# Optimization experiments

Hardware: AMD Instinct MI355X
Metric: run time of the kernel (lower is better)

## Reference

```python
import jax, jax.numpy as jnp
import numpy as np

S1, S2, B, H, E, IN, OUT, NL = 8, 32, 256, 1024, 512, 2, 2, 4


def setup_inputs() -> dict:
    key = jax.random.key(0)
    ks = jax.random.split(key, 20)
    s_h = 1.0 / np.sqrt(H)
    inp = {
        'input': jax.random.normal(ks[0], (B, IN), jnp.float32),
        'h0': jax.random.normal(ks[1], (NL, B, H), jnp.float32) * 0.5,
        'c0': jax.random.normal(ks[2], (NL, B, H), jnp.float32) * 0.5,
        'all_outputs': jax.random.normal(ks[3], (S1, S2, B, H), jnp.float32),
        'W_emb': jax.random.normal(ks[4], (E, IN), jnp.float32) / np.sqrt(IN),
        'b_emb': jax.random.normal(ks[5], (E,), jnp.float32) * 0.01,
        'W_attn': jax.random.normal(ks[6], (1, 2 * H), jnp.float32) / np.sqrt(2 * H),
        'b_attn': jax.random.normal(ks[7], (1,), jnp.float32) * 0.01,
        'Wih0': jax.random.normal(ks[8], (4 * H, E + H), jnp.float32) / np.sqrt(E + H),
        'Whh0': jax.random.normal(ks[9], (4 * H, H), jnp.float32) * s_h,
        'bih0': jax.random.normal(ks[10], (4 * H,), jnp.float32) * 0.01,
        'bhh0': jax.random.normal(ks[11], (4 * H,), jnp.float32) * 0.01,
        'Wih_r': jax.random.normal(ks[12], (NL - 1, 4 * H, H), jnp.float32) * s_h,
        'Whh_r': jax.random.normal(ks[13], (NL - 1, 4 * H, H), jnp.float32) * s_h,
        'bih_r': jax.random.normal(ks[14], (NL - 1, 4 * H), jnp.float32) * 0.01,
        'bhh_r': jax.random.normal(ks[15], (NL - 1, 4 * H), jnp.float32) * 0.01,
        'W_out': jax.random.normal(ks[16], (OUT, H), jnp.float32) * s_h,
        'b_out': jax.random.normal(ks[17], (OUT,), jnp.float32) * 0.01,
    }
    return inp


def _lstm_cell(x, h, c, Wih, Whh, bih, bhh):
    g = x @ Wih.T + h @ Whh.T + bih + bhh  # [B, 4H], torch gate order i,f,g,o
    i, f, gg, o = jnp.split(g, 4, axis=1)
    c2 = jax.nn.sigmoid(f) * c + jax.nn.sigmoid(i) * jnp.tanh(gg)
    h2 = jax.nn.sigmoid(o) * jnp.tanh(c2)
    return h2, c2


def reference(input, h0, c0, all_outputs, W_emb, b_emb, W_attn, b_attn,
              Wih0, Whh0, bih0, bhh0, Wih_r, Whh_r, bih_r, bhh_r, W_out, b_out):
    s1, s2, b, h_dim = all_outputs.shape
    # embedding (dropout = identity in eval mode)
    embedded = jax.nn.relu(input @ W_emb.T + b_emb)  # [B, E]
    h_top = h0[0]  # [B, H]
    # attn(cat(h_top, y)) decomposed: h part is shared across all (j, i)
    w_h = W_attn[0, :h_dim]
    w_y = W_attn[0, h_dim:]
    scores = (jnp.einsum('jibh,h->jib', all_outputs, w_y)
              + (h_top @ w_h)[None, None, :] + b_attn[0])  # [S1, S2, B]
    # torch cats per-(j,i) [B,1] columns j-major -> [B, S1*S2]
    normalized = jax.nn.softmax(scores.reshape(s1 * s2, b).T, axis=1)  # [B, S1*S2]
    temp = normalized.reshape(b, s1, s2)
    # NOTE: original writes into an expand()-ed zero buffer, so every j-slice
    # aliases the same memory; after the loop all slices equal the last j's bmm
    # result and sum(0) multiplies it by S1. We replicate that exactly.
    applied_last = jnp.einsum('bi,ibh->bh', temp[:, -1, :], all_outputs[-1])  # [B, H]
    final_attn = s1 * applied_last
    x = jnp.concatenate([final_attn, embedded], axis=1)  # [B, H+E]
    hs, cs = [], []
    h, c = _lstm_cell(x, h0[0], c0[0], Wih0, Whh0, bih0, bhh0)
    hs.append(h); cs.append(c)
    for l in range(Wih_r.shape[0]):  # inter-layer dropout = identity in eval
        h, c = _lstm_cell(h, h0[l + 1], c0[l + 1], Wih_r[l], Whh_r[l], bih_r[l], bhh_r[l])
        hs.append(h); cs.append(c)
    h_new = jnp.stack(hs)
    c_new = jnp.stack(cs)
    final_output = h @ W_out.T + b_out  # [B, OUT]
    return final_output, h_new, c_new, normalized
```

## Files before the change

kernel.cpp:

```cpp
#include <hip/hip_runtime.h>
#include <hip/hip_bf16.h>

typedef __bf16 bf16x8 __attribute__((ext_vector_type(8)));
typedef __bf16 bf16x4 __attribute__((ext_vector_type(4)));
typedef float  f32x4  __attribute__((ext_vector_type(4)));

#define O_FINAL 0
#define O_H     512
#define O_C     1049088
#define O_NORM  2097664

__device__ __forceinline__ bf16x8 cvt8(float4 a, float4 b) {
  bf16x8 r;
  r[0] = (__bf16)a.x; r[1] = (__bf16)a.y; r[2] = (__bf16)a.z; r[3] = (__bf16)a.w;
  r[4] = (__bf16)b.x; r[5] = (__bf16)b.y; r[6] = (__bf16)b.z; r[7] = (__bf16)b.w;
  return r;
}

template<int K>
__device__ __forceinline__ void tile_gemm_ff(const float* __restrict__ A,
                                             const float* __restrict__ W,
                                             int r0, int j0,
                                             __bf16* __restrict__ At,
                                             __bf16* __restrict__ Wt,
                                             f32x4 acc[2]) {
  const int t = threadIdx.x, lane = t & 63, wave = t >> 6;
  const int rf = wave & 3, gg = wave >> 2;
  const int tr = t >> 3, chunk = t & 7;
  const float* wsrc = W + (size_t)((tr >> 4) * 1024 + j0 + (tr & 15)) * K + chunk * 8;
  const float* asrc = A + (size_t)(r0 + tr) * K + chunk * 8;
  const int sw_off = (chunk ^ (tr & 7)) << 4;
  char* wdst = (char*)Wt + tr * 128 + sw_off;
  char* adst = (char*)At + tr * 128 + sw_off;
  const int a_tr  = rf * 16 + (lane & 15);
  const int w_tr0 = gg * 32 + (lane & 15);
  const int w_tr1 = w_tr0 + 16;
  const int ksel  = lane >> 4;

  float4 wr0 = *(const float4*)wsrc, wr1 = *(const float4*)(wsrc + 4);
  float4 ar0 = *(const float4*)asrc, ar1 = *(const float4*)(asrc + 4);

  constexpr int NK = K / 64;
#pragma unroll 2
  for (int step = 0; step < NK; ++step) {
    __syncthreads();
    *(bf16x8*)wdst = cvt8(wr0, wr1);
    *(bf16x8*)adst = cvt8(ar0, ar1);
    __syncthreads();
    if (step + 1 < NK) {
      wr0 = *(const float4*)(wsrc + (step + 1) * 64);
      wr1 = *(const float4*)(wsrc + (step + 1) * 64 + 4);
      ar0 = *(const float4*)(asrc + (step + 1) * 64);
      ar1 = *(const float4*)(asrc + (step + 1) * 64 + 4);
    }
#pragma unroll
    for (int s = 0; s < 2; ++s) {
      const int chk = s * 4 + ksel;
      bf16x8 af  = *(const bf16x8*)((char*)At + a_tr  * 128 + ((chk ^ (a_tr  & 7)) << 4));
      bf16x8 wf0 = *(const bf16x8*)((char*)Wt + w_tr0 * 128 + ((chk ^ (w_tr0 & 7)) << 4));
      bf16x8 wf1 = *(const bf16x8*)((char*)Wt + w_tr1 * 128 + ((chk ^ (w_tr1 & 7)) << 4));
      acc[0] = __builtin_amdgcn_mfma_f32_16x16x32_bf16(af, wf0, acc[0], 0, 0, 0);
      acc[1] = __builtin_amdgcn_mfma_f32_16x16x32_bf16(af, wf1, acc[1], 0, 0, 0);
    }
  }
}

template<int K>
__device__ __forceinline__ void tile_gemm_bb(const __bf16* __restrict__ A,
                                             const __bf16* __restrict__ W,
                                             int r0, int j0,
                                             __bf16* __restrict__ At,
                                             __bf16* __restrict__ Wt,
                                             f32x4 acc[2]) {
  const int t = threadIdx.x, lane = t & 63, wave = t >> 6;
  const int rf = wave & 3, gg = wave >> 2;
  const int tr = t >> 3, chunk = t & 7;
  const __bf16* wsrc = W + (size_t)((tr >> 4) * 1024 + j0 + (tr & 15)) * K + chunk * 8;
  const __bf16* asrc = A + (size_t)(r0 + tr) * K + chunk * 8;
  const int sw_off = (chunk ^ (tr & 7)) << 4;
  char* wdst = (char*)Wt + tr * 128 + sw_off;
  char* adst = (char*)At + tr * 128 + sw_off;
  const int a_tr  = rf * 16 + (lane & 15);
  const int w_tr0 = gg * 32 + (lane & 15);
  const int w_tr1 = w_tr0 + 16;
  const int ksel  = lane >> 4;

  bf16x8 wr = *(const bf16x8*)wsrc;
  bf16x8 ar = *(const bf16x8*)asrc;

  constexpr int NK = K / 64;
#pragma unroll 2
  for (int step = 0; step < NK; ++step) {
    __syncthreads();
    *(bf16x8*)wdst = wr;
    *(bf16x8*)adst = ar;
    __syncthreads();
    if (step + 1 < NK) {
      wr = *(const bf16x8*)(wsrc + (step + 1) * 64);
      ar = *(const bf16x8*)(asrc + (step + 1) * 64);
    }
#pragma unroll
    for (int s = 0; s < 2; ++s) {
      const int chk = s * 4 + ksel;
      bf16x8 af  = *(const bf16x8*)((char*)At + a_tr  * 128 + ((chk ^ (a_tr  & 7)) << 4));
      bf16x8 wf0 = *(const bf16x8*)((char*)Wt + w_tr0 * 128 + ((chk ^ (w_tr0 & 7)) << 4));
      bf16x8 wf1 = *(const bf16x8*)((char*)Wt + w_tr1 * 128 + ((chk ^ (w_tr1 & 7)) << 4));
      acc[0] = __builtin_amdgcn_mfma_f32_16x16x32_bf16(af, wf0, acc[0], 0, 0, 0);
      acc[1] = __builtin_amdgcn_mfma_f32_16x16x32_bf16(af, wf1, acc[1], 0, 0, 0);
    }
  }
}

__global__ __launch_bounds__(512) void k_front(
    const float* __restrict__ AO, const float* __restrict__ Wattn,
    float* __restrict__ sc,
    const float* __restrict__ h0,
    const float* __restrict__ Whh0, const float* __restrict__ Whh_r,
    const float* __restrict__ bih0, const float* __restrict__ bhh0,
    const float* __restrict__ bih_r, const float* __restrict__ bhh_r,
    float* __restrict__ Gh,
    const float* __restrict__ Wih0, const float* __restrict__ Wih_r,
    __bf16* __restrict__ Wihb) {
  const int t = threadIdx.x, lane = t & 63, wave = t >> 6;
  if (blockIdx.x < 2048) {
    const float* wy = Wattn + 1024;
    float4 wv[4];
#pragma unroll
    for (int q = 0; q < 4; ++q) wv[q] = *(const float4*)(wy + lane * 4 + 256 * q);
    const int row0 = (blockIdx.x * 8 + wave) * 4;
    float a4[4];
#pragma unroll
    for (int rr = 0; rr < 4; ++rr) {
      const float4* rp = (const float4*)(AO + (size_t)(row0 + rr) * 1024);
      float a = 0.f;
#pragma unroll
      for (int q = 0; q < 4; ++q) {
        float4 v = rp[lane + 64 * q];
        a += v.x * wv[q].x + v.y * wv[q].y + v.z * wv[q].z + v.w * wv[q].w;
      }
      a4[rr] = a;
    }
#pragma unroll
    for (int rr = 0; rr < 4; ++rr) {
      float a = a4[rr];
#pragma unroll
      for (int off = 32; off; off >>= 1) a += __shfl_xor(a, off, 64);
      if (lane == 0) {
        int row = row0 + rr;
        sc[(row & 255) * 256 + (row >> 8)] = a;
      }
    }
    return;
  }
  if (blockIdx.x < 3072) {
    __shared__ __bf16 At[64 * 64];
    __shared__ __bf16 Wt[64 * 64];
    const int j = blockIdx.x - 2048;
    const int l = j >> 8, inner = j & 255;
    const int cb = inner & 63, rb = inner >> 6;
    const int j0 = cb * 16, r0 = rb * 64;
    const float* A  = h0 + (size_t)l * 262144;
    const float* W  = (l == 0) ? Whh0 : (Whh_r + (size_t)(l - 1) * 4194304);
    const float* bi = (l == 0) ? bih0 : (bih_r + (size_t)(l - 1) * 4096);
    const float* bh = (l == 0) ? bhh0 : (bhh_r + (size_t)(l - 1) * 4096);
    f32x4 acc[2] = {};
    tile_gemm_ff<1024>(A, W, r0, j0, At, Wt, acc);
    float* Go = Gh + (size_t)l * 1048576;
    const int rf = wave & 3, gg = wave >> 2;
    const int col = j0 + (lane & 15);
    const int rbase = r0 + rf * 16 + ((lane >> 4) << 2);
#pragma unroll
    for (int gi = 0; gi < 2; ++gi) {
      const int cg = (gg * 2 + gi) * 1024 + col;
#pragma unroll
      for (int q = 0; q < 4; ++q)
        Go[(size_t)(rbase + q) * 4096 + cg] = acc[gi][q] + bi[cg] + bh[cg];
    }
    return;
  }
  const int tid = ((int)blockIdx.x - 3072) * 512 + t;
#pragma unroll
  for (int n = 0; n < 8; ++n) {
    int idx = tid + n * 589824;
    float4 v = (idx < 1572864) ? ((const float4*)Wih0)[idx]
                               : ((const float4*)Wih_r)[idx - 1572864];
    bf16x4 o;
    o[0] = (__bf16)v.x; o[1] = (__bf16)v.y; o[2] = (__bf16)v.z; o[3] = (__bf16)v.w;
    ((bf16x4*)Wihb)[idx] = o;
  }
}

__global__ __launch_bounds__(256) void k_smx(const float* __restrict__ sc,
                                             const float* __restrict__ AO,
                                             const float* __restrict__ inp,
                                             const float* __restrict__ Wemb,
                                             const float* __restrict__ bemb,
                                             float* __restrict__ norm_out,
                                             __bf16* __restrict__ x) {
  __shared__ float red[4];
  __shared__ float wsm[32];
  const int b = blockIdx.x, t = threadIdx.x, lane = t & 63, wave = t >> 6;
  float s = sc[b * 256 + t];
  float m = s;
#pragma unroll
  for (int off = 32; off; off >>= 1) m = fmaxf(m, __shfl_xor(m, off, 64));
  if (lane == 0) red[wave] = m;
  __syncthreads();
  m = fmaxf(fmaxf(red[0], red[1]), fmaxf(red[2], red[3]));
  float e = __expf(s - m);
  float sum = e;
#pragma unroll
  for (int off = 32; off; off >>= 1) sum += __shfl_xor(sum, off, 64);
  __syncthreads();
  if (lane == 0) red[wave] = sum;
  __syncthreads();
  sum = red[0] + red[1] + red[2] + red[3];
  float nv = e / sum;
  norm_out[b * 256 + t] = nv;
  if (t >= 224) wsm[t - 224] = nv;
  __syncthreads();
  float acc[4] = {0.f, 0.f, 0.f, 0.f};
  const float* base = AO + ((size_t)224 * 256 + b) * 1024;
#pragma unroll 4
  for (int i = 0; i < 32; ++i) {
    float w = wsm[i];
    const float* rp = base + (size_t)i * 262144;
#pragma unroll
    for (int q = 0; q < 4; ++q) acc[q] += w * rp[t + 256 * q];
  }
#pragma unroll
  for (int q = 0; q < 4; ++q) x[(size_t)b * 1536 + t + 256 * q] = (__bf16)(8.0f * acc[q]);
  float i0 = inp[b * 2], i1 = inp[b * 2 + 1];
#pragma unroll
  for (int r = 0; r < 2; ++r) {
    int jj = t + 256 * r;
    float e2 = i0 * Wemb[jj * 2] + i1 * Wemb[jj * 2 + 1] + bemb[jj];
    x[(size_t)b * 1536 + 1024 + jj] = (__bf16)fmaxf(e2, 0.f);
  }
}

template<int K>
__global__ __launch_bounds__(512) void k_layer(const __bf16* __restrict__ A,
                                               const __bf16* __restrict__ Wb,
                                               const float* __restrict__ Gh,
                                               const float* __restrict__ c0l,
                                               float* __restrict__ h_out,
                                               float* __restrict__ c_out,
                                               __bf16* __restrict__ hb) {
  __shared__ __bf16 At[64 * 64];
  __shared__ __bf16 Wt[64 * 64];
  __shared__ float exch[4][2][256];
  const int t = threadIdx.x, lane = t & 63, wave = t >> 6;
  const int rf = wave & 3, gg = wave >> 2;
  const int cb = blockIdx.x & 63, rb = blockIdx.x >> 6;
  const int j0 = cb * 16, r0 = rb * 64;
  f32x4 acc[2] = {};
  tile_gemm_bb<K>(A, Wb, r0, j0, At, Wt, acc);
  const int col = j0 + (lane & 15);
  const int rbase = r0 + rf * 16 + ((lane >> 4) << 2);
#pragma unroll
  for (int gi = 0; gi < 2; ++gi) {
    const float* gp = Gh + (size_t)rbase * 4096 + (gg * 2 + gi) * 1024 + col;
#pragma unroll
    for (int q = 0; q < 4; ++q) acc[gi][q] += gp[(size_t)q * 4096];
  }
  const int eidx = ((lane >> 4) << 2) * 16 + (lane & 15);
  if (gg == 1) {
#pragma unroll
    for (int gi = 0; gi < 2; ++gi)
#pragma unroll
      for (int q = 0; q < 4; ++q)
        exch[rf][gi][eidx + q * 16] = acc[gi][q];
  }
  __syncthreads();
  if (gg == 0) {
#pragma unroll
    for (int q = 0; q < 4; ++q) {
      const int row = rbase + q;
      float gv = exch[rf][0][eidx + q * 16];
      float ov = exch[rf][1][eidx + q * 16];
      float si = 1.f / (1.f + __expf(-acc[0][q]));
      float sf = 1.f / (1.f + __expf(-acc[1][q]));
      float so = 1.f / (1.f + __expf(-ov));
      float c2 = sf * c0l[(size_t)row * 1024 + col] + si * tanhf(gv);
      float h2 = so * tanhf(c2);
      h_out[(size_t)row * 1024 + col] = h2;
      c_out[(size_t)row * 1024 + col] = c2;
      hb[(size_t)row * 1024 + col] = (__bf16)h2;
    }
  }
}

__global__ __launch_bounds__(256) void k_final(const float* __restrict__ h3,
                                               const float* __restrict__ Wout,
                                               const float* __restrict__ bout,
                                               float* __restrict__ out) {
  const int lane = threadIdx.x & 63, wave = threadIdx.x >> 6;
  const int b = blockIdx.x * 4 + wave;
  const float4* hp = (const float4*)(h3 + (size_t)b * 1024);
  const float4* w0 = (const float4*)Wout;
  const float4* w1 = (const float4*)(Wout + 1024);
  float a0 = 0.f, a1 = 0.f;
#pragma unroll
  for (int q = 0; q < 4; ++q) {
    float4 hv = hp[lane + 64 * q];
    float4 v0 = w0[lane + 64 * q];
    float4 v1 = w1[lane + 64 * q];
    a0 += hv.x * v0.x + hv.y * v0.y + hv.z * v0.z + hv.w * v0.w;
    a1 += hv.x * v1.x + hv.y * v1.y + hv.z * v1.z + hv.w * v1.w;
  }
#pragma unroll
  for (int off = 32; off; off >>= 1) {
    a0 += __shfl_xor(a0, off, 64);
    a1 += __shfl_xor(a1, off, 64);
  }
  if (lane == 0) {
    out[b * 2]     = a0 + bout[0];
    out[b * 2 + 1] = a1 + bout[1];
  }
}

extern "C" void kernel_launch(void* const* d_in, const int* in_sizes, int n_in,
                              void* d_out, int out_size, void* d_ws, size_t ws_size,
                              hipStream_t stream) {
  const float* inp    = (const float*)d_in[0];
  const float* h0     = (const float*)d_in[1];
  const float* c0     = (const float*)d_in[2];
  const float* AO     = (const float*)d_in[3];
  const float* Wemb   = (const float*)d_in[4];
  const float* bemb   = (const float*)d_in[5];
  const float* Wattn  = (const float*)d_in[6];
  const float* Wih0   = (const float*)d_in[8];
  const float* Whh0   = (const float*)d_in[9];
  const float* bih0   = (const float*)d_in[10];
  const float* bhh0   = (const float*)d_in[11];
  const float* Wih_r  = (const float*)d_in[12];
  const float* Whh_r  = (const float*)d_in[13];
  const float* bih_r  = (const float*)d_in[14];
  const float* bhh_r  = (const float*)d_in[15];
  const float* Wout   = (const float*)d_in[16];
  const float* bout   = (const float*)d_in[17];

  float* out = (float*)d_out;
  char* ws = (char*)d_ws;

  __bf16* Wihb  = (__bf16*)ws;
  float*  Gh    = (float*)(ws + 37748736);
  __bf16* xb    = (__bf16*)(ws + 54525952);
  __bf16* hb    = (__bf16*)(ws + 55312384);
  float*  sc    = (float*)(ws + 57409536);
  __bf16* Wihb0 = Wihb;
  __bf16* Wihbr = Wihb + 6291456;

  k_front<<<4224, 512, 0, stream>>>(AO, Wattn, sc, h0, Whh0, Whh_r,
                                    bih0, bhh0, bih_r, bhh_r, Gh,
                                    Wih0, Wih_r, Wihb);
  k_smx<<<256, 256, 0, stream>>>(sc, AO, inp, Wemb, bemb, out + O_NORM, xb);

  k_layer<1536><<<256, 512, 0, stream>>>(xb, Wihb0, Gh, c0,
                                         out + O_H, out + O_C, hb);
  for (int l = 1; l < 4; ++l)
    k_layer<1024><<<256, 512, 0, stream>>>(hb + (size_t)(l - 1) * 262144,
                                           Wihbr + (size_t)(l - 1) * 4194304,
                                           Gh + (size_t)l * 1048576,
                                           c0 + (size_t)l * 262144,
                                           out + O_H + (size_t)l * 262144,
                                           out + O_C + (size_t)l * 262144,
                                           hb + (size_t)l * 262144);

  k_final<<<64, 256, 0, stream>>>(out + O_H + 3 * 262144, Wout, bout, out + O_FINAL);
}
```

Before: 166.3 us.

## Double-buffer LDS tiles and prefetch four K-steps ahead in GEMM tiles

Reworks both tile GEMM helpers to use two LDS buffers with a single barrier per K-step, and keeps four register-staged global loads in flight instead of one. The goal is to hide global memory latency and drop one barrier per iteration in the recurrent-weight GEMM and the per-layer LSTM GEMMs. The cost is more registers for the prefetch slots and a larger shared buffer of 40 KB per block, which may reduce occupancy. The exch area now sits inside the shared buffer, so an extra barrier guards its reuse.

```diff
diff --git a/kernel.cpp b/kernel.cpp
--- a/kernel.cpp
+++ b/kernel.cpp
@@ -18,93 +18,101 @@
 }
 
 template<int K>
+__device__ __forceinline__ void tile_gemm_bb(const __bf16* __restrict__ A,
+                                             const __bf16* __restrict__ W,
+                                             int r0, int j0, char* lds,
+                                             f32x4 acc[2]) {
+  constexpr int NK = K / 64;
+  constexpr int D = 4;
+  const int t = threadIdx.x, lane = t & 63, wave = t >> 6;
+  const int rf = wave & 3, gg = wave >> 2;
+  const int tr = t >> 3, chunk = t & 7;
+  const __bf16* wsrc = W + (size_t)((tr >> 4) * 1024 + j0 + (tr & 15)) * K + chunk * 8;
+  const __bf16* asrc = A + (size_t)(r0 + tr) * K + chunk * 8;
+  const int sw_off = (chunk ^ (tr & 7)) << 4;
+  const int woff = 8192 + tr * 128 + sw_off;
+  const int aoff = tr * 128 + sw_off;
+  const int a_tr  = rf * 16 + (lane & 15);
+  const int w_tr0 = gg * 32 + (lane & 15);
+  const int w_tr1 = w_tr0 + 16;
+  const int ksel  = lane >> 4;
+
+  bf16x8 wp[D], ap[D];
+#pragma unroll
+  for (int d = 0; d < D; ++d) {
+    wp[d] = *(const bf16x8*)(wsrc + d * 64);
+    ap[d] = *(const bf16x8*)(asrc + d * 64);
+  }
+#pragma unroll
+  for (int s = 0; s < NK; ++s) {
+    const int sl = s % D;
+    char* buf = lds + (s & 1) * 16384;
+    *(bf16x8*)(buf + aoff) = ap[sl];
+    *(bf16x8*)(buf + woff) = wp[sl];
+    if (s + D < NK) {
+      wp[sl] = *(const bf16x8*)(wsrc + (s + D) * 64);
+      ap[sl] = *(const bf16x8*)(asrc + (s + D) * 64);
+    }
+    __syncthreads();
+#pragma unroll
+    for (int s2 = 0; s2 < 2; ++s2) {
+      const int chk = s2 * 4 + ksel;
+      bf16x8 af  = *(const bf16x8*)(buf + a_tr * 128 + ((chk ^ (a_tr & 7)) << 4));
+      bf16x8 wf0 = *(const bf16x8*)(buf + 8192 + w_tr0 * 128 + ((chk ^ (w_tr0 & 7)) << 4));
+      bf16x8 wf1 = *(const bf16x8*)(buf + 8192 + w_tr1 * 128 + ((chk ^ (w_tr1 & 7)) << 4));
+      acc[0] = __builtin_amdgcn_mfma_f32_16x16x32_bf16(af, wf0, acc[0], 0, 0, 0);
+      acc[1] = __builtin_amdgcn_mfma_f32_16x16x32_bf16(af, wf1, acc[1], 0, 0, 0);
+    }
+  }
+}
+
+template<int K>
 __device__ __forceinline__ void tile_gemm_ff(const float* __restrict__ A,
                                              const float* __restrict__ W,
-                                             int r0, int j0,
-                                             __bf16* __restrict__ At,
-                                             __bf16* __restrict__ Wt,
+                                             int r0, int j0, char* lds,
                                              f32x4 acc[2]) {
+  constexpr int NK = K / 64;
+  constexpr int D = 4;
   const int t = threadIdx.x, lane = t & 63, wave = t >> 6;
   const int rf = wave & 3, gg = wave >> 2;
   const int tr = t >> 3, chunk = t & 7;
   const float* wsrc = W + (size_t)((tr >> 4) * 1024 + j0 + (tr & 15)) * K + chunk * 8;
   const float* asrc = A + (size_t)(r0 + tr) * K + chunk * 8;
   const int sw_off = (chunk ^ (tr & 7)) << 4;
-  char* wdst = (char*)Wt + tr * 128 + sw_off;
-  char* adst = (char*)At + tr * 128 + sw_off;
+  const int woff = 8192 + tr * 128 + sw_off;
+  const int aoff = tr * 128 + sw_off;
   const int a_tr  = rf * 16 + (lane & 15);
   const int w_tr0 = gg * 32 + (lane & 15);
   const int w_tr1 = w_tr0 + 16;
   const int ksel  = lane >> 4;
 
-  float4 wr0 = *(const float4*)wsrc, wr1 = *(const float4*)(wsrc + 4);
-  float4 ar0 = *(const float4*)asrc, ar1 = *(const float4*)(asrc + 4);
-
-  constexpr int NK = K / 64;
-#pragma unroll 2
-  for (int step = 0; step < NK; ++step) {
+  float4 wp[D][2], ap[D][2];
+#pragma unroll
+  for (int d = 0; d < D; ++d) {
+    wp[d][0] = *(const float4*)(wsrc + d * 64);
+    wp[d][1] = *(const float4*)(wsrc + d * 64 + 4);
+    ap[d][0] = *(const float4*)(asrc + d * 64);
+    ap[d][1] = *(const float4*)(asrc + d * 64 + 4);
+  }
+#pragma unroll
+  for (int s = 0; s < NK; ++s) {
+    const int sl = s % D;
+    char* buf = lds + (s & 1) * 16384;
+    *(bf16x8*)(buf + aoff) = cvt8(ap[sl][0], ap[sl][1]);
+    *(bf16x8*)(buf + woff) = cvt8(wp[sl][0], wp[sl][1]);
+    if (s + D < NK) {
+      wp[sl][0] = *(const float4*)(wsrc + (s + D) * 64);
+      wp[sl][1] = *(const float4*)(wsrc + (s + D) * 64 + 4);
+      ap[sl][0] = *(const float4*)(asrc + (s + D) * 64);
+      ap[sl][1] = *(const float4*)(asrc + (s + D) * 64 + 4);
+    }
     __syncthreads();
-    *(bf16x8*)wdst = cvt8(wr0, wr1);
-    *(bf16x8*)adst = cvt8(ar0, ar1);
-    __syncthreads();
-    if (step + 1 < NK) {
-      wr0 = *(const float4*)(wsrc + (step + 1) * 64);
-      wr1 = *(const float4*)(wsrc + (step + 1) * 64 + 4);
-      ar0 = *(const float4*)(asrc + (step + 1) * 64);
-      ar1 = *(const float4*)(asrc + (step + 1) * 64 + 4);
-    }
-#pragma unroll
-    for (int s = 0; s < 2; ++s) {
-      const int chk = s * 4 + ksel;
-      bf16x8 af  = *(const bf16x8*)((char*)At + a_tr  * 128 + ((chk ^ (a_tr  & 7)) << 4));
-      bf16x8 wf0 = *(const bf16x8*)((char*)Wt + w_tr0 * 128 + ((chk ^ (w_tr0 & 7)) << 4));
-      bf16x8 wf1 = *(const bf16x8*)((char*)Wt + w_tr1 * 128 + ((chk ^ (w_tr1 & 7)) << 4));
-      acc[0] = __builtin_amdgcn_mfma_f32_16x16x32_bf16(af, wf0, acc[0], 0, 0, 0);
-      acc[1] = __builtin_amdgcn_mfma_f32_16x16x32_bf16(af, wf1, acc[1], 0, 0, 0);
-    }
-  }
-}
-
-template<int K>
-__device__ __forceinline__ void tile_gemm_bb(const __bf16* __restrict__ A,
-                                             const __bf16* __restrict__ W,
-                                             int r0, int j0,
-                                             __bf16* __restrict__ At,
-                                             __bf16* __restrict__ Wt,
-                                             f32x4 acc[2]) {
-  const int t = threadIdx.x, lane = t & 63, wave = t >> 6;
-  const int rf = wave & 3, gg = wave >> 2;
-  const int tr = t >> 3, chunk = t & 7;
-  const __bf16* wsrc = W + (size_t)((tr >> 4) * 1024 + j0 + (tr & 15)) * K + chunk * 8;
-  const __bf16* asrc = A + (size_t)(r0 + tr) * K + chunk * 8;
-  const int sw_off = (chunk ^ (tr & 7)) << 4;
-  char* wdst = (char*)Wt + tr * 128 + sw_off;
-  char* adst = (char*)At + tr * 128 + sw_off;
-  const int a_tr  = rf * 16 + (lane & 15);
-  const int w_tr0 = gg * 32 + (lane & 15);
-  const int w_tr1 = w_tr0 + 16;
-  const int ksel  = lane >> 4;
-
-  bf16x8 wr = *(const bf16x8*)wsrc;
-  bf16x8 ar = *(const bf16x8*)asrc;
-
-  constexpr int NK = K / 64;
-#pragma unroll 2
-  for (int step = 0; step < NK; ++step) {
-    __syncthreads();
-    *(bf16x8*)wdst = wr;
-    *(bf16x8*)adst = ar;
-    __syncthreads();
-    if (step + 1 < NK) {
-      wr = *(const bf16x8*)(wsrc + (step + 1) * 64);
-      ar = *(const bf16x8*)(asrc + (step + 1) * 64);
-    }
-#pragma unroll
-    for (int s = 0; s < 2; ++s) {
-      const int chk = s * 4 + ksel;
-      bf16x8 af  = *(const bf16x8*)((char*)At + a_tr  * 128 + ((chk ^ (a_tr  & 7)) << 4));
-      bf16x8 wf0 = *(const bf16x8*)((char*)Wt + w_tr0 * 128 + ((chk ^ (w_tr0 & 7)) << 4));
-      bf16x8 wf1 = *(const bf16x8*)((char*)Wt + w_tr1 * 128 + ((chk ^ (w_tr1 & 7)) << 4));
+#pragma unroll
+    for (int s2 = 0; s2 < 2; ++s2) {
+      const int chk = s2 * 4 + ksel;
+      bf16x8 af  = *(const bf16x8*)(buf + a_tr * 128 + ((chk ^ (a_tr & 7)) << 4));
+      bf16x8 wf0 = *(const bf16x8*)(buf + 8192 + w_tr0 * 128 + ((chk ^ (w_tr0 & 7)) << 4));
+      bf16x8 wf1 = *(const bf16x8*)(buf + 8192 + w_tr1 * 128 + ((chk ^ (w_tr1 & 7)) << 4));
       acc[0] = __builtin_amdgcn_mfma_f32_16x16x32_bf16(af, wf0, acc[0], 0, 0, 0);
       acc[1] = __builtin_amdgcn_mfma_f32_16x16x32_bf16(af, wf1, acc[1], 0, 0, 0);
     }
@@ -153,8 +161,7 @@
     return;
   }
   if (blockIdx.x < 3072) {
-    __shared__ __bf16 At[64 * 64];
-    __shared__ __bf16 Wt[64 * 64];
+    __shared__ char smem[40960];
     const int j = blockIdx.x - 2048;
     const int l = j >> 8, inner = j & 255;
     const int cb = inner & 63, rb = inner >> 6;
@@ -164,7 +171,7 @@
     const float* bi = (l == 0) ? bih0 : (bih_r + (size_t)(l - 1) * 4096);
     const float* bh = (l == 0) ? bhh0 : (bhh_r + (size_t)(l - 1) * 4096);
     f32x4 acc[2] = {};
-    tile_gemm_ff<1024>(A, W, r0, j0, At, Wt, acc);
+    tile_gemm_ff<1024>(A, W, r0, j0, smem, acc);
     float* Go = Gh + (size_t)l * 1048576;
     const int rf = wave & 3, gg = wave >> 2;
     const int col = j0 + (lane & 15);
@@ -247,15 +254,14 @@
                                                float* __restrict__ h_out,
                                                float* __restrict__ c_out,
                                                __bf16* __restrict__ hb) {
-  __shared__ __bf16 At[64 * 64];
-  __shared__ __bf16 Wt[64 * 64];
-  __shared__ float exch[4][2][256];
+  __shared__ char smem[40960];
+  float* exch = (float*)(smem + 32768);
   const int t = threadIdx.x, lane = t & 63, wave = t >> 6;
   const int rf = wave & 3, gg = wave >> 2;
   const int cb = blockIdx.x & 63, rb = blockIdx.x >> 6;
   const int j0 = cb * 16, r0 = rb * 64;
   f32x4 acc[2] = {};
-  tile_gemm_bb<K>(A, Wb, r0, j0, At, Wt, acc);
+  tile_gemm_bb<K>(A, Wb, r0, j0, smem, acc);
   const int col = j0 + (lane & 15);
   const int rbase = r0 + rf * 16 + ((lane >> 4) << 2);
 #pragma unroll
@@ -265,20 +271,21 @@
     for (int q = 0; q < 4; ++q) acc[gi][q] += gp[(size_t)q * 4096];
   }
   const int eidx = ((lane >> 4) << 2) * 16 + (lane & 15);
+  __syncthreads();
   if (gg == 1) {
 #pragma unroll
     for (int gi = 0; gi < 2; ++gi)
 #pragma unroll
       for (int q = 0; q < 4; ++q)
-        exch[rf][gi][eidx + q * 16] = acc[gi][q];
+        exch[(rf * 2 + gi) * 256 + eidx + q * 16] = acc[gi][q];
   }
   __syncthreads();
   if (gg == 0) {
 #pragma unroll
     for (int q = 0; q < 4; ++q) {
       const int row = rbase + q;
-      float gv = exch[rf][0][eidx + q * 16];
-      float ov = exch[rf][1][eidx + q * 16];
+      float gv = exch[(rf * 2 + 0) * 256 + eidx + q * 16];
+      float ov = exch[(rf * 2 + 1) * 256 + eidx + q * 16];
       float si = 1.f / (1.f + __expf(-acc[0][q]));
       float sf = 1.f / (1.f + __expf(-acc[1][q]));
       float so = 1.f / (1.f + __expf(-ov));
```

After: 154.1 us. -7.4%, faster.
